# Optimization experiments

Hardware: AMD Instinct MI355X
Metric: run time of the kernel (lower is better)

The kernel has to match this reference:

```python
import jax, jax.numpy as jnp
import numpy as np

B, Q, C = 2, 8192, 256
L, P, NH = 4, 4, 8
DH = C // NH
HMAX = 128  # max level resolution; smaller levels are zero-padded (mimics sparse COO extents)


def _inverse_sigmoid(x, eps=1e-5):
    x = jnp.clip(x, 0.0, 1.0)
    return jnp.log(jnp.clip(x, eps, None) / jnp.clip(1.0 - x, eps, None))


def setup_inputs() -> dict:
    key = jax.random.key(0)
    ks = jax.random.split(key, 8)
    query = jax.random.normal(ks[0], (Q, C), jnp.float32)
    xy_reference_points = jax.random.uniform(ks[1], (Q, 2), dtype=jnp.float32)
    spatial_shapes = jnp.array([[128, 128], [64, 64], [32, 32], [16, 16]], jnp.int32)
    values = jax.random.normal(ks[2], (B, HMAX, HMAX, L, C), jnp.float32)
    # zero out entries outside each level's (H_l, W_l) extent, like the sparse COO tensor
    ys = jnp.arange(HMAX)[:, None, None]
    xs = jnp.arange(HMAX)[None, :, None]
    mask = (ys < spatial_shapes[:, 0]) & (xs < spatial_shapes[:, 1])  # [HMAX, HMAX, L]
    values = values * mask[None, :, :, :, None]
    batch_offsets = jnp.array([0, Q // B], jnp.int32)
    s = 0.02
    W_so = jax.random.normal(ks[3], (L * P * NH * 2, C), jnp.float32) * s
    b_so = jax.random.normal(ks[4], (L * P * NH * 2,), jnp.float32) * 0.5
    W_aw = jax.random.normal(ks[5], (L * P * NH, C), jnp.float32) * s
    b_aw = jnp.zeros((L * P * NH,), jnp.float32)
    W_v = jax.random.normal(ks[6], (C, C), jnp.float32) * s
    b_v = jnp.zeros((C,), jnp.float32)
    W_o = jax.random.normal(ks[7], (C, C), jnp.float32) * s
    b_o = jnp.zeros((C,), jnp.float32)
    return dict(query=query, xy_reference_points=xy_reference_points, values=values,
                W_so=W_so, b_so=b_so, W_aw=W_aw, b_aw=b_aw, W_v=W_v, b_v=b_v,
                W_o=W_o, b_o=b_o, batch_offsets=batch_offsets, spatial_shapes=spatial_shapes)


def _forward(query, ref, values, W_so, b_so, W_aw, b_aw, W_v, b_v, W_o, b_o,
             batch_offsets, spatial_shapes):
    # value projection applied to (sparse) feature values, then split heads
    v = values @ W_v.T + b_v                      # [B, HMAX, HMAX, L, C]
    v = v.reshape(B, HMAX, HMAX, L, NH, DH)
    # sampling offsets and attention weights from queries
    offs = (query @ W_so.T + b_so).reshape(Q, L, P, NH, 2)
    aw = jax.nn.softmax((query @ W_aw.T + b_aw).reshape(Q, L * P, NH), axis=1)
    aw = aw.reshape(Q, L, P, NH)
    # sampling locations in (0,1), then grid_sample convention (align_corners=False)
    loc = jax.nn.sigmoid(_inverse_sigmoid(ref)[:, None, None, None, :] + offs)  # [Q,L,P,NH,2]
    g = loc * 2.0 - 1.0
    Hs = spatial_shapes[:, 0].astype(jnp.float32)[None, :, None, None]
    Ws = spatial_shapes[:, 1].astype(jnp.float32)[None, :, None, None]
    x = (g[..., 0] + 1.0) * Ws * 0.5 - 0.5        # [Q,L,P,NH] pixel coords
    y = (g[..., 1] + 1.0) * Hs * 0.5 - 0.5
    x0f = jnp.floor(x); y0f = jnp.floor(y)
    wx1 = x - x0f; wx0 = 1.0 - wx1
    wy1 = y - y0f; wy0 = 1.0 - wy1
    x0 = x0f.astype(jnp.int32); y0 = y0f.astype(jnp.int32)
    x1 = x0 + 1; y1 = y0 + 1
    # per-query batch index from batch_offsets
    b_idx = (jnp.searchsorted(batch_offsets, jnp.arange(Q), side='right') - 1)[:, None, None, None]
    l_idx = jnp.arange(L)[None, :, None, None]
    h_idx = jnp.arange(NH)[None, None, None, :]
    Hsi = spatial_shapes[:, 0][None, :, None, None]
    Wsi = spatial_shapes[:, 1][None, :, None, None]

    def corner(yi, xi):
        valid = (xi >= 0) & (xi < Wsi) & (yi >= 0) & (yi < Hsi)
        xc = jnp.clip(xi, 0, HMAX - 1)
        yc = jnp.clip(yi, 0, HMAX - 1)
        vals = v[b_idx, yc, xc, l_idx, h_idx]     # [Q, L, P, NH, DH]
        return vals * valid[..., None]

    sampled = (corner(y0, x0) * (wy0 * wx0)[..., None]
               + corner(y0, x1) * (wy0 * wx1)[..., None]
               + corner(y1, x0) * (wy1 * wx0)[..., None]
               + corner(y1, x1) * (wy1 * wx1)[..., None])  # [Q, L, P, NH, DH]
    out = jnp.einsum('qlphd,qlph->qhd', sampled, aw).reshape(Q, C)
    return out @ W_o.T + b_o


def reference(query, xy_reference_points, values, W_so, b_so, W_aw, b_aw,
              W_v, b_v, W_o, b_o, batch_offsets, spatial_shapes):
    return _forward(query, xy_reference_points, values, W_so, b_so, W_aw, b_aw,
                    W_v, b_v, W_o, b_o, batch_offsets, spatial_shapes)
```

## Files before the change

### kernel.cpp

```cpp
#include <hip/hip_runtime.h>
#include <math.h>

#define QTOT   8192
#define LNUM   4
#define PNUM   4
#define NHEAD  8
#define DHEAD  32
#define HMAX   128
#define NV_PER_B 21760
#define MROWS  (2 * NV_PER_B)
#define QPERB  4096

#define G1_MT  (MROWS / 128)
#define G1_BLKS (G1_MT * 2)
#define G2_BLKS (128 * 3)

typedef __attribute__((ext_vector_type(8))) short bf16x8;
typedef __attribute__((ext_vector_type(4))) float f32x4;

static __device__ __forceinline__ ushort bf16_hi(float f) {
    return (ushort)(__builtin_bit_cast(unsigned int, f) >> 16);
}
static __device__ __forceinline__ ushort bf16_lo(float f, ushort hi) {
    float hf = __builtin_bit_cast(float, ((unsigned int)hi) << 16);
    return (ushort)(__builtin_bit_cast(unsigned int, f - hf) >> 16);
}
static __device__ __forceinline__ ushort bf16_rne(float f) {
    unsigned u = __builtin_bit_cast(unsigned int, f);
    unsigned rr = (u + 0x7FFFu + ((u >> 16) & 1u)) >> 16;
    return (ushort)rr;
}

template<int GATHER, int BM, int NPROD, int OUTBF16>
__device__ __forceinline__
void gemm_body(const float* __restrict__ A,
               const float* __restrict__ B1,
               const float* __restrict__ B2,
               const float* __restrict__ bias1,
               const float* __restrict__ bias2,
               void* __restrict__ Out,
               int nsplit, int ldo, int bx, int by, char* smem)
{
    constexpr int MI  = BM / 32;
    constexpr int AIT = BM * 8 / 256;
    constexpr int PL  = (NPROD > 1) ? 2 : 1;
    ushort* sAp = (ushort*)smem;
    ushort* sBp = sAp + 2 * PL * BM * 32;
    int* rowBase = (int*)(sBp + 2 * PL * 128 * 32);

    const int tid = threadIdx.x;
    const int m0 = bx * BM;
    const int n0 = by * 128;

    if (GATHER) {
        for (int s = tid; s < BM; s += 256) {
            int r = m0 + s;
            int b = (r >= NV_PER_B) ? 1 : 0;
            int rp = r - b * NV_PER_B;
            int l, y, x;
            if (rp < 16384)      { l = 0; y = rp >> 7; x = rp & 127; }
            else if (rp < 20480) { int rr = rp - 16384; l = 1; y = rr >> 6; x = rr & 63; }
            else if (rp < 21504) { int rr = rp - 20480; l = 2; y = rr >> 5; x = rr & 31; }
            else                 { int rr = rp - 21504; l = 3; y = rr >> 4; x = rr & 15; }
            rowBase[s] = (((((b << 7) | y) << 7) | x) * 4 + l) << 8;
        }
        __syncthreads();
    }

    float4 pa[AIT], pb[4];

    auto loadA = [&](int kt) {
        #pragma unroll
        for (int i = 0; i < AIT; ++i) {
            int s = tid + i * 256;
            int r = s >> 3, c4 = s & 7;
            const float* src = GATHER
                ? A + rowBase[r] + kt * 32 + c4 * 4
                : A + (size_t)(m0 + r) * 256 + kt * 32 + c4 * 4;
            pa[i] = *(const float4*)src;
        }
        #pragma unroll
        for (int i = 0; i < 4; ++i) {
            int s = tid + i * 256;
            int r = s >> 3, c4 = s & 7;
            int bn = n0 + r;
            const float* src = ((bn < nsplit) ? B1 + (size_t)bn * 256
                                              : B2 + (size_t)(bn - nsplit) * 256)
                               + kt * 32 + c4 * 4;
            pb[i] = *(const float4*)src;
        }
    };

    auto writeLDS = [&](int buf) {
        #pragma unroll
        for (int i = 0; i < AIT; ++i) {
            int s = tid + i * 256;
            int r = s >> 3, c4 = s & 7;
            float4 v = pa[i];
            ushort4 hi;
            hi.x = bf16_hi(v.x); hi.y = bf16_hi(v.y);
            hi.z = bf16_hi(v.z); hi.w = bf16_hi(v.w);
            int idx = r * 32 + ((((c4 >> 1) ^ (r & 3)) << 3) | ((c4 & 1) << 2));
            *(ushort4*)&sAp[(buf * PL + 0) * BM * 32 + idx] = hi;
            if (NPROD > 1) {
                ushort4 lo;
                lo.x = bf16_lo(v.x, hi.x); lo.y = bf16_lo(v.y, hi.y);
                lo.z = bf16_lo(v.z, hi.z); lo.w = bf16_lo(v.w, hi.w);
                *(ushort4*)&sAp[(buf * PL + PL - 1) * BM * 32 + idx] = lo;
            }
        }
        #pragma unroll
        for (int i = 0; i < 4; ++i) {
            int s = tid + i * 256;
            int r = s >> 3, c4 = s & 7;
            float4 v = pb[i];
            ushort4 hi;
            hi.x = bf16_hi(v.x); hi.y = bf16_hi(v.y);
            hi.z = bf16_hi(v.z); hi.w = bf16_hi(v.w);
            int idx = r * 32 + ((((c4 >> 1) ^ (r & 3)) << 3) | ((c4 & 1) << 2));
            *(ushort4*)&sBp[(buf * PL + 0) * 128 * 32 + idx] = hi;
            if (NPROD > 1) {
                ushort4 lo;
                lo.x = bf16_lo(v.x, hi.x); lo.y = bf16_lo(v.y, hi.y);
                lo.z = bf16_lo(v.z, hi.z); lo.w = bf16_lo(v.w, hi.w);
                *(ushort4*)&sBp[(buf * PL + PL - 1) * 128 * 32 + idx] = lo;
            }
        }
    };

    const int lane = tid & 63;
    const int wid  = tid >> 6;
    const int wrow = (wid >> 1) * (BM / 2);
    const int wcol = (wid & 1) * 64;
    const int fr   = lane & 15;
    const int ks   = lane >> 4;

    f32x4 acc[MI][4] = {};

    loadA(0);
    writeLDS(0);

    for (int kt = 0; kt < 8; ++kt) {
        __syncthreads();
        if (kt < 7) loadA(kt + 1);

        const int buf = kt & 1;
        bf16x8 ah[MI], al[MI], bh[4], bl[4];
        #pragma unroll
        for (int mi = 0; mi < MI; ++mi) {
            int row = wrow + mi * 16 + fr;
            int idx = row * 32 + ((ks ^ (row & 3)) << 3);
            ah[mi] = *(const bf16x8*)&sAp[(buf * PL + 0) * BM * 32 + idx];
            if (NPROD > 1) al[mi] = *(const bf16x8*)&sAp[(buf * PL + PL - 1) * BM * 32 + idx];
        }
        #pragma unroll
        for (int ni = 0; ni < 4; ++ni) {
            int row = wcol + ni * 16 + fr;
            int idx = row * 32 + ((ks ^ (row & 3)) << 3);
            bh[ni] = *(const bf16x8*)&sBp[(buf * PL + 0) * 128 * 32 + idx];
            if (NPROD > 1) bl[ni] = *(const bf16x8*)&sBp[(buf * PL + PL - 1) * 128 * 32 + idx];
        }
        #pragma unroll
        for (int mi = 0; mi < MI; ++mi)
            #pragma unroll
            for (int ni = 0; ni < 4; ++ni) {
                acc[mi][ni] = __builtin_amdgcn_mfma_f32_16x16x32_bf16(ah[mi], bh[ni], acc[mi][ni], 0, 0, 0);
                if (NPROD > 1) {
                    acc[mi][ni] = __builtin_amdgcn_mfma_f32_16x16x32_bf16(ah[mi], bl[ni], acc[mi][ni], 0, 0, 0);
                    acc[mi][ni] = __builtin_amdgcn_mfma_f32_16x16x32_bf16(al[mi], bh[ni], acc[mi][ni], 0, 0, 0);
                }
            }

        if (kt < 7) writeLDS((kt + 1) & 1);
    }

    #pragma unroll
    for (int mi = 0; mi < MI; ++mi)
        #pragma unroll
        for (int ni = 0; ni < 4; ++ni) {
            int col = n0 + wcol + ni * 16 + fr;
            float bs = (col < nsplit) ? bias1[col] : bias2[col - nsplit];
            int rbase = m0 + wrow + mi * 16 + ks * 4;
            #pragma unroll
            for (int rr = 0; rr < 4; ++rr) {
                float val = acc[mi][ni][rr] + bs;
                if (OUTBF16)
                    ((ushort*)Out)[(size_t)(rbase + rr) * ldo + col] = bf16_rne(val);
                else
                    ((float*)Out)[(size_t)(rbase + rr) * ldo + col] = val;
            }
        }
}

__global__ __launch_bounds__(256)
void fused_g12(const float* __restrict__ values,
               const float* __restrict__ W_v,  const float* __restrict__ b_v,
               const float* __restrict__ query,
               const float* __restrict__ W_so, const float* __restrict__ W_aw,
               const float* __restrict__ b_so, const float* __restrict__ b_aw,
               ushort* __restrict__ vproj, float* __restrict__ qbuf)
{
    extern __shared__ char smem[];
    const int f = blockIdx.x;
    if (f < G1_BLKS) {
        gemm_body<1, 128, 1, 1>(values, W_v, W_v, b_v, b_v, vproj,
                                256, 256, f % G1_MT, f / G1_MT, smem);
    } else {
        const int g = f - G1_BLKS;
        gemm_body<0, 64, 3, 0>(query, W_so, W_aw, b_so, b_aw, qbuf,
                               256, 384, g % 128, g / 128, smem);
    }
}

__global__ __launch_bounds__(256)
void gemm_o(const float* __restrict__ mid,
            const float* __restrict__ W_o, const float* __restrict__ b_o,
            float* __restrict__ out)
{
    extern __shared__ char smem[];
    gemm_body<0, 64, 1, 0>(mid, W_o, W_o, b_o, b_o, out,
                           256, 256, blockIdx.x, blockIdx.y, smem);
}

__global__ __launch_bounds__(256)
void sample4(const ushort* __restrict__ vproj,
             const float* __restrict__ qbuf,
             const float* __restrict__ ref,
             float* __restrict__ mid)
{
    __shared__ int   s_row[4][128][4];
    __shared__ float s_w[4][128][4];
    __shared__ float s_logit[4][16][8];
    __shared__ float s_aw[4][16][8];

    const int tid = threadIdx.x;
    const int q0 = blockIdx.x * 4;

    #pragma unroll
    for (int it = 0; it < 2; ++it) {
        const int cc = tid + it * 256;
        const int qq = cc >> 7, c = cc & 127;
        const int q = q0 + qq;
        const int b = (q >= QPERB) ? 1 : 0;
        const int lp = c >> 3, l = lp >> 2;
        const float offx = qbuf[(size_t)q * 384 + c * 2 + 0];
        const float offy = qbuf[(size_t)q * 384 + c * 2 + 1];
        float rx = fminf(fmaxf(ref[q * 2 + 0], 0.f), 1.f);
        float ry = fminf(fmaxf(ref[q * 2 + 1], 0.f), 1.f);
        const float eps = 1e-5f;
        const float isx = logf(fmaxf(rx, eps) / fmaxf(1.f - rx, eps));
        const float isy = logf(fmaxf(ry, eps) / fmaxf(1.f - ry, eps));
        const float locx = 1.f / (1.f + expf(-(isx + offx)));
        const float locy = 1.f / (1.f + expf(-(isy + offy)));
        const int Wl = HMAX >> l, Hl = HMAX >> l;
        const float x = locx * (float)Wl - 0.5f;
        const float y = locy * (float)Hl - 0.5f;
        const float x0f = floorf(x), y0f = floorf(y);
        const float wx1 = x - x0f, wx0 = 1.f - wx1;
        const float wy1 = y - y0f, wy0 = 1.f - wy1;
        const int x0 = (int)x0f, y0 = (int)y0f;
        const int lo = (l == 0) ? 0 : (l == 1) ? 16384 : (l == 2) ? 20480 : 21504;
        const int base = b * NV_PER_B + lo;
        const int   xs[2] = {x0, x0 + 1};
        const int   ys[2] = {y0, y0 + 1};
        const float wxs[2] = {wx0, wx1};
        const float wys[2] = {wy0, wy1};
        #pragma unroll
        for (int cy = 0; cy < 2; ++cy)
            #pragma unroll
            for (int cx = 0; cx < 2; ++cx) {
                const int xi = xs[cx], yi = ys[cy];
                const bool valid = (xi >= 0) & (xi < Wl) & (yi >= 0) & (yi < Hl);
                const int idx = cy * 2 + cx;
                s_row[qq][c][idx] = valid ? (base + yi * Wl + xi) : 0;
                s_w[qq][c][idx]   = valid ? (wys[cy] * wxs[cx]) : 0.f;
            }
        s_logit[qq][lp][c & 7] = qbuf[(size_t)q * 384 + 256 + c];
    }
    __syncthreads();

    if (tid < 32) {
        const int qq = tid >> 3, h = tid & 7;
        float m = -INFINITY;
        #pragma unroll
        for (int j = 0; j < 16; ++j) m = fmaxf(m, s_logit[qq][j][h]);
        float s = 0.f;
        #pragma unroll
        for (int j = 0; j < 16; ++j) s += expf(s_logit[qq][j][h] - m);
        const float inv = 1.f / s;
        #pragma unroll
        for (int j = 0; j < 16; ++j)
            s_aw[qq][j][h] = expf(s_logit[qq][j][h] - m) * inv;
    }
    __syncthreads();

    const int qq = tid >> 6, t6 = tid & 63;
    const int h = t6 >> 3, d4 = t6 & 7;
    const int q = q0 + qq;
    float ax = 0.f, ay = 0.f, az = 0.f, aw_ = 0.f;
    #pragma unroll
    for (int lp = 0; lp < 16; ++lp) {
        const int c = lp * 8 + h;
        const float aw = s_aw[qq][lp][h];
        float sx = 0.f, sy = 0.f, sz = 0.f, sw = 0.f;
        #pragma unroll
        for (int j = 0; j < 4; ++j) {
            const int row = s_row[qq][c][j];
            const float w = s_w[qq][c][j];
            const uint2 u = *(const uint2*)&vproj[(size_t)row * 256 + h * 32 + d4 * 4];
            const float v0 = __builtin_bit_cast(float, u.x << 16);
            const float v1 = __builtin_bit_cast(float, u.x & 0xFFFF0000u);
            const float v2 = __builtin_bit_cast(float, u.y << 16);
            const float v3 = __builtin_bit_cast(float, u.y & 0xFFFF0000u);
            sx = fmaf(w, v0, sx); sy = fmaf(w, v1, sy);
            sz = fmaf(w, v2, sz); sw = fmaf(w, v3, sw);
        }
        ax = fmaf(aw, sx, ax); ay = fmaf(aw, sy, ay);
        az = fmaf(aw, sz, az); aw_ = fmaf(aw, sw, aw_);
    }
    float4 o = {ax, ay, az, aw_};
    *(float4*)&mid[(size_t)q * 256 + t6 * 4] = o;
}

extern "C" void kernel_launch(void* const* d_in, const int* in_sizes, int n_in,
                              void* d_out, int out_size, void* d_ws, size_t ws_size,
                              hipStream_t stream)
{
    const float* query  = (const float*)d_in[0];
    const float* ref    = (const float*)d_in[1];
    const float* values = (const float*)d_in[2];
    const float* W_so   = (const float*)d_in[3];
    const float* b_so   = (const float*)d_in[4];
    const float* W_aw   = (const float*)d_in[5];
    const float* b_aw   = (const float*)d_in[6];
    const float* W_v    = (const float*)d_in[7];
    const float* b_v    = (const float*)d_in[8];
    const float* W_o    = (const float*)d_in[9];
    const float* b_o    = (const float*)d_in[10];
    float* out = (float*)d_out;

    ushort* vproj = (ushort*)d_ws;
    float* qbuf  = (float*)d_ws + ((size_t)MROWS * 256 * 2) / 4;
    float* mid   = qbuf + (size_t)QTOT * 384;

    const int smem_bytes = 48 * 1024 + 1024;

    dim3 blk(256);
    fused_g12<<<dim3(G1_BLKS + G2_BLKS), blk, smem_bytes, stream>>>(
        values, W_v, b_v, query, W_so, W_aw, b_so, b_aw, vproj, qbuf);
    sample4<<<dim3(QTOT / 4), blk, 0, stream>>>(vproj, qbuf, ref, mid);
    gemm_o<<<dim3(QTOT / 64, 2), blk, smem_bytes, stream>>>(mid, W_o, b_o, out);
}
```

Before: 263.0 us.

## Sample one query per block with 16-byte gathers and shuffle reduction

The sampling kernel now handles one query per 256-thread block instead of four. Threads are spread across corners and sampling points, and each lane loads 8 bf16 values with a single 16-byte load rather than 4 values with 8 bytes. Partial sums are combined with cross-lane xor shuffles. The softmax attention weight is folded into the bilinear corner weights in shared memory ahead of the gather, and row and weight are packed into one int2. This aims to raise memory-level parallelism in the gather loop, at the cost of four times as many blocks, an extra barrier, and the shuffle reduction.

```diff
diff --git a/kernel.cpp b/kernel.cpp
--- a/kernel.cpp
+++ b/kernel.cpp
@@ -223,35 +223,31 @@
 }
 
 __global__ __launch_bounds__(256)
-void sample4(const ushort* __restrict__ vproj,
+void sample1(const ushort* __restrict__ vproj,
              const float* __restrict__ qbuf,
              const float* __restrict__ ref,
              float* __restrict__ mid)
 {
-    __shared__ int   s_row[4][128][4];
-    __shared__ float s_w[4][128][4];
-    __shared__ float s_logit[4][16][8];
-    __shared__ float s_aw[4][16][8];
+    __shared__ int2  s_rw[128][4];
+    __shared__ float s_logit[16][8];
+    __shared__ float s_aw[16][8];
 
     const int tid = threadIdx.x;
-    const int q0 = blockIdx.x * 4;
-
-    #pragma unroll
-    for (int it = 0; it < 2; ++it) {
-        const int cc = tid + it * 256;
-        const int qq = cc >> 7, c = cc & 127;
-        const int q = q0 + qq;
-        const int b = (q >= QPERB) ? 1 : 0;
-        const int lp = c >> 3, l = lp >> 2;
-        const float offx = qbuf[(size_t)q * 384 + c * 2 + 0];
-        const float offy = qbuf[(size_t)q * 384 + c * 2 + 1];
+    const int q = blockIdx.x;
+    const int b = (q >= QPERB) ? 1 : 0;
+
+    if (tid < 128) {
+        const int c  = tid;
+        const int lp = c >> 3;
+        const int l  = lp >> 2;
+        const float2 off = *(const float2*)&qbuf[(size_t)q * 384 + c * 2];
         float rx = fminf(fmaxf(ref[q * 2 + 0], 0.f), 1.f);
         float ry = fminf(fmaxf(ref[q * 2 + 1], 0.f), 1.f);
         const float eps = 1e-5f;
         const float isx = logf(fmaxf(rx, eps) / fmaxf(1.f - rx, eps));
         const float isy = logf(fmaxf(ry, eps) / fmaxf(1.f - ry, eps));
-        const float locx = 1.f / (1.f + expf(-(isx + offx)));
-        const float locy = 1.f / (1.f + expf(-(isy + offy)));
+        const float locx = 1.f / (1.f + expf(-(isx + off.x)));
+        const float locy = 1.f / (1.f + expf(-(isy + off.y)));
         const int Wl = HMAX >> l, Hl = HMAX >> l;
         const float x = locx * (float)Wl - 0.5f;
         const float y = locy * (float)Hl - 0.5f;
@@ -272,54 +268,75 @@
                 const int xi = xs[cx], yi = ys[cy];
                 const bool valid = (xi >= 0) & (xi < Wl) & (yi >= 0) & (yi < Hl);
                 const int idx = cy * 2 + cx;
-                s_row[qq][c][idx] = valid ? (base + yi * Wl + xi) : 0;
-                s_w[qq][c][idx]   = valid ? (wys[cy] * wxs[cx]) : 0.f;
-            }
-        s_logit[qq][lp][c & 7] = qbuf[(size_t)q * 384 + 256 + c];
+                s_rw[c][idx].x = valid ? (base + yi * Wl + xi) : 0;
+                s_rw[c][idx].y = __float_as_int(valid ? (wys[cy] * wxs[cx]) : 0.f);
+            }
+        s_logit[lp][c & 7] = qbuf[(size_t)q * 384 + 256 + c];
     }
     __syncthreads();
 
-    if (tid < 32) {
-        const int qq = tid >> 3, h = tid & 7;
+    if (tid < 8) {
+        const int h = tid;
         float m = -INFINITY;
         #pragma unroll
-        for (int j = 0; j < 16; ++j) m = fmaxf(m, s_logit[qq][j][h]);
+        for (int j = 0; j < 16; ++j) m = fmaxf(m, s_logit[j][h]);
         float s = 0.f;
         #pragma unroll
-        for (int j = 0; j < 16; ++j) s += expf(s_logit[qq][j][h] - m);
+        for (int j = 0; j < 16; ++j) s += expf(s_logit[j][h] - m);
         const float inv = 1.f / s;
         #pragma unroll
         for (int j = 0; j < 16; ++j)
-            s_aw[qq][j][h] = expf(s_logit[qq][j][h] - m) * inv;
+            s_aw[j][h] = expf(s_logit[j][h] - m) * inv;
     }
     __syncthreads();
 
-    const int qq = tid >> 6, t6 = tid & 63;
-    const int h = t6 >> 3, d4 = t6 & 7;
-    const int q = q0 + qq;
-    float ax = 0.f, ay = 0.f, az = 0.f, aw_ = 0.f;
     #pragma unroll
-    for (int lp = 0; lp < 16; ++lp) {
+    for (int t2 = tid; t2 < 512; t2 += 256) {
+        const int c = t2 >> 2, j = t2 & 3;
+        const float aw = s_aw[c >> 3][c & 7];
+        s_rw[c][j].y = __float_as_int(__int_as_float(s_rw[c][j].y) * aw);
+    }
+    __syncthreads();
+
+    const int h  = tid >> 5;
+    const int l5 = tid & 31;
+    const int ds = l5 & 3;
+    const int rt = l5 >> 2;
+    const int j  = rt & 3;
+    const int rtH = rt >> 2;
+
+    float a0 = 0.f, a1 = 0.f, a2 = 0.f, a3 = 0.f;
+    float a4 = 0.f, a5 = 0.f, a6 = 0.f, a7 = 0.f;
+    #pragma unroll
+    for (int it = 0; it < 8; ++it) {
+        const int lp = 2 * it + rtH;
         const int c = lp * 8 + h;
-        const float aw = s_aw[qq][lp][h];
-        float sx = 0.f, sy = 0.f, sz = 0.f, sw = 0.f;
-        #pragma unroll
-        for (int j = 0; j < 4; ++j) {
-            const int row = s_row[qq][c][j];
-            const float w = s_w[qq][c][j];
-            const uint2 u = *(const uint2*)&vproj[(size_t)row * 256 + h * 32 + d4 * 4];
-            const float v0 = __builtin_bit_cast(float, u.x << 16);
-            const float v1 = __builtin_bit_cast(float, u.x & 0xFFFF0000u);
-            const float v2 = __builtin_bit_cast(float, u.y << 16);
-            const float v3 = __builtin_bit_cast(float, u.y & 0xFFFF0000u);
-            sx = fmaf(w, v0, sx); sy = fmaf(w, v1, sy);
-            sz = fmaf(w, v2, sz); sw = fmaf(w, v3, sw);
-        }
-        ax = fmaf(aw, sx, ax); ay = fmaf(aw, sy, ay);
-        az = fmaf(aw, sz, az); aw_ = fmaf(aw, sw, aw_);
-    }
-    float4 o = {ax, ay, az, aw_};
-    *(float4*)&mid[(size_t)q * 256 + t6 * 4] = o;
+        const int2 rw = s_rw[c][j];
+        const float w = __int_as_float(rw.y);
+        const uint4 u = *(const uint4*)&vproj[(size_t)rw.x * 256 + h * 32 + ds * 8];
+        a0 = fmaf(w, __builtin_bit_cast(float, u.x << 16), a0);
+        a1 = fmaf(w, __builtin_bit_cast(float, u.x & 0xFFFF0000u), a1);
+        a2 = fmaf(w, __builtin_bit_cast(float, u.y << 16), a2);
+        a3 = fmaf(w, __builtin_bit_cast(float, u.y & 0xFFFF0000u), a3);
+        a4 = fmaf(w, __builtin_bit_cast(float, u.z << 16), a4);
+        a5 = fmaf(w, __builtin_bit_cast(float, u.z & 0xFFFF0000u), a5);
+        a6 = fmaf(w, __builtin_bit_cast(float, u.w << 16), a6);
+        a7 = fmaf(w, __builtin_bit_cast(float, u.w & 0xFFFF0000u), a7);
+    }
+    #pragma unroll
+    for (int m = 4; m <= 16; m <<= 1) {
+        a0 += __shfl_xor(a0, m); a1 += __shfl_xor(a1, m);
+        a2 += __shfl_xor(a2, m); a3 += __shfl_xor(a3, m);
+        a4 += __shfl_xor(a4, m); a5 += __shfl_xor(a5, m);
+        a6 += __shfl_xor(a6, m); a7 += __shfl_xor(a7, m);
+    }
+    if (rt == 0) {
+        float* dst = &mid[(size_t)q * 256 + h * 32 + ds * 8];
+        float4 o0 = {a0, a1, a2, a3};
+        float4 o1 = {a4, a5, a6, a7};
+        *(float4*)dst = o0;
+        *(float4*)(dst + 4) = o1;
+    }
 }
 
 extern "C" void kernel_launch(void* const* d_in, const int* in_sizes, int n_in,
@@ -348,6 +365,6 @@
     dim3 blk(256);
     fused_g12<<<dim3(G1_BLKS + G2_BLKS), blk, smem_bytes, stream>>>(
         values, W_v, b_v, query, W_so, W_aw, b_so, b_aw, vproj, qbuf);
-    sample4<<<dim3(QTOT / 4), blk, 0, stream>>>(vproj, qbuf, ref, mid);
+    sample1<<<dim3(QTOT), blk, 0, stream>>>(vproj, qbuf, ref, mid);
     gemm_o<<<dim3(QTOT / 64, 2), blk, smem_bytes, stream>>>(mid, W_o, b_o, out);
 }
```

Result: no change. 266.6 us (+1.4%).
